# Kernel optimization log

Hardware: AMD Instinct MI355X
Metric: run time of the kernel (lower is better)

Reference implementation:

```python
import jax, jax.numpy as jnp
import numpy as np

N_NODES = 100000
N_EDGES = 1600000
IN_C, HID, OUT_C = 128, 128, 64
BN_EPS = 1e-5


def gcn_conv(x, W, b, src, dst):
    # PyG GCNConv(normalize=False): linear first, then sum-aggregate over edges
    m = x @ W                                   # [N, out_dim]
    agg = jax.ops.segment_sum(m[src], dst, num_segments=N_NODES)  # scatter-add by dst
    return agg + b


def batch_norm(h, gamma, beta):
    mu = jnp.mean(h, axis=0)
    var = jnp.var(h, axis=0)
    return (h - mu) * jax.lax.rsqrt(var + BN_EPS) * gamma + beta


def setup_inputs() -> dict:
    key = jax.random.key(0)
    ks = jax.random.split(key, 8)
    x = jax.random.normal(ks[0], (N_NODES, IN_C), dtype=jnp.float32)
    edge_src = jax.random.randint(ks[1], (N_EDGES,), 0, N_NODES, dtype=jnp.int32)
    edge_dst = jnp.sort(jax.random.randint(ks[2], (N_EDGES,), 0, N_NODES, dtype=jnp.int32))
    def glorot(k, shape):
        lim = float(np.sqrt(6.0 / (shape[0] + shape[1])))
        return jax.random.uniform(k, shape, jnp.float32, -lim, lim)
    return {
        "x": x, "edge_src": edge_src, "edge_dst": edge_dst,
        "W0": glorot(ks[3], (IN_C, HID)), "b0": jnp.zeros((HID,), jnp.float32),
        "W1": glorot(ks[4], (HID, HID)), "b1": jnp.zeros((HID,), jnp.float32),
        "W2": glorot(ks[5], (HID, OUT_C)), "b2": jnp.zeros((OUT_C,), jnp.float32),
        "g0": jnp.ones((HID,), jnp.float32), "be0": jnp.zeros((HID,), jnp.float32),
        "g1": jnp.ones((HID,), jnp.float32), "be1": jnp.zeros((HID,), jnp.float32),
    }


def reference(x, edge_src, edge_dst, W0, b0, W1, b1, W2, b2, g0, be0, g1, be1):
    # layer 0: conv -> BN -> residual (dims match: 128==128) -> ReLU (dropout p=0)
    h = gcn_conv(x, W0, b0, edge_src, edge_dst)
    h = batch_norm(h, g0, be0)
    h = h + x  # residual, in_channels == hidden_channels
    x1 = jax.nn.relu(h)
    # layer 1
    h = gcn_conv(x1, W1, b1, edge_src, edge_dst)
    h = batch_norm(h, g1, be1)
    h = h + x1
    x2 = jax.nn.relu(h)
    # final layer: conv only
    return gcn_conv(x2, W2, b2, edge_src, edge_dst)
```

## Files before the change

### kernel.cpp

```cpp
#include <hip/hip_runtime.h>

#define BN_EPS 1e-5f

typedef __attribute__((ext_vector_type(8))) short bf16x8;
typedef __attribute__((ext_vector_type(4))) float f32x4;

__device__ __forceinline__ short f2bf(float f) {
    union { float f; unsigned u; } v; v.f = f;
    unsigned r = (v.u + 0x7fffu + ((v.u >> 16) & 1u)) >> 16;
    return (short)r;
}
__device__ __forceinline__ float bflo(unsigned d) {
    union { unsigned u; float f; } v; v.u = d << 16; return v.f;
}
__device__ __forceinline__ float bfhi(unsigned d) {
    union { unsigned u; float f; } v; v.u = d & 0xffff0000u; return v.f;
}

__global__ __launch_bounds__(256) void build_off_k(const int* __restrict__ dst,
                                                   int* __restrict__ off, int E, int N) {
    int i = blockIdx.x * 256 + threadIdx.x;
    if (i > E) return;
    int cur  = (i < E) ? dst[i] : N;
    int prev = (i == 0) ? -1 : dst[i - 1];
    for (int n = prev + 1; n <= cur; ++n) off[n] = i;
}

__global__ void zero_k(float* p, int n) {
    int i = blockIdx.x * blockDim.x + threadIdx.x;
    if (i < n) p[i] = 0.f;
}

__global__ __launch_bounds__(256) void wtrans_k(const float* __restrict__ W,
                                                short* __restrict__ Wt, int K, int C) {
    int i = blockIdx.x * 256 + threadIdx.x;
    if (i >= K * C) return;
    int c = i / K, k = i % K;
    Wt[i] = f2bf(W[k * C + c]);
}

template <int OUTC, int MODE>
__global__ __launch_bounds__(256) void mgemm_k(const void* __restrict__ Xp,
                                               const short* __restrict__ Wt,
                                               short* __restrict__ M,
                                               const float* __restrict__ ss,
                                               const void* __restrict__ Rp,
                                               short* __restrict__ X1, int N) {
    constexpr int NR = OUTC / 16;
    __shared__ short sW[OUTC][136];

    const int tid = threadIdx.x;
    for (int q = tid; q < OUTC * 16; q += 256) {
        int r = q >> 4, s = q & 15;
        *(int4*)&sW[r][s * 8] = ((const int4*)Wt)[q];
    }
    __syncthreads();

    const int wave = tid >> 6, lane = tid & 63;
    const int lr = lane & 15, lg = lane >> 4;
    const int row0 = blockIdx.x * 128 + wave * 32;

    f32x4 acc[2][NR];
    #pragma unroll
    for (int m = 0; m < 2; ++m)
        #pragma unroll
        for (int n = 0; n < NR; ++n) acc[m][n] = (f32x4){0.f, 0.f, 0.f, 0.f};

    #pragma unroll
    for (int kk = 0; kk < 4; ++kk) {
        bf16x8 a[2];
        const int ch0 = kk * 32 + lg * 8;
        #pragma unroll
        for (int m = 0; m < 2; ++m) {
            int row = row0 + m * 16 + lr;
            float v[8] = {0.f, 0.f, 0.f, 0.f, 0.f, 0.f, 0.f, 0.f};
            if (row < N) {
                if constexpr (MODE == 0) {
                    const float4* p = (const float4*)((const float*)Xp + (size_t)row * 128 + ch0);
                    float4 h0 = p[0], h1 = p[1];
                    v[0] = h0.x; v[1] = h0.y; v[2] = h0.z; v[3] = h0.w;
                    v[4] = h1.x; v[5] = h1.y; v[6] = h1.z; v[7] = h1.w;
                } else {
                    int4 hb = *(const int4*)((const short*)Xp + (size_t)row * 128 + ch0);
                    v[0] = bflo(hb.x); v[1] = bfhi(hb.x);
                    v[2] = bflo(hb.y); v[3] = bfhi(hb.y);
                    v[4] = bflo(hb.z); v[5] = bfhi(hb.z);
                    v[6] = bflo(hb.w); v[7] = bfhi(hb.w);
                    float4 sc0 = *(const float4*)&ss[ch0];
                    float4 sc1 = *(const float4*)&ss[ch0 + 4];
                    float4 sh0 = *(const float4*)&ss[128 + ch0];
                    float4 sh1 = *(const float4*)&ss[128 + ch0 + 4];
                    float sc[8] = {sc0.x, sc0.y, sc0.z, sc0.w, sc1.x, sc1.y, sc1.z, sc1.w};
                    float sh[8] = {sh0.x, sh0.y, sh0.z, sh0.w, sh1.x, sh1.y, sh1.z, sh1.w};
                    float r[8];
                    if constexpr (MODE == 1) {
                        const float4* rp = (const float4*)((const float*)Rp + (size_t)row * 128 + ch0);
                        float4 r0 = rp[0], r1 = rp[1];
                        r[0] = r0.x; r[1] = r0.y; r[2] = r0.z; r[3] = r0.w;
                        r[4] = r1.x; r[5] = r1.y; r[6] = r1.z; r[7] = r1.w;
                    } else {
                        int4 rb = *(const int4*)((const short*)Rp + (size_t)row * 128 + ch0);
                        r[0] = bflo(rb.x); r[1] = bfhi(rb.x);
                        r[2] = bflo(rb.y); r[3] = bfhi(rb.y);
                        r[4] = bflo(rb.z); r[5] = bfhi(rb.z);
                        r[6] = bflo(rb.w); r[7] = bfhi(rb.w);
                    }
                    #pragma unroll
                    for (int k = 0; k < 8; ++k)
                        v[k] = fmaxf(fmaf(v[k], sc[k], sh[k]) + r[k], 0.f);
                }
            }
            #pragma unroll
            for (int k = 0; k < 8; ++k) a[m][k] = f2bf(v[k]);
            if constexpr (MODE == 1) {
                if (row < N) *(bf16x8*)&X1[(size_t)row * 128 + ch0] = a[m];
            }
        }
        #pragma unroll
        for (int n = 0; n < NR; ++n) {
            bf16x8 b = *(const bf16x8*)&sW[n * 16 + lr][kk * 32 + lg * 8];
            acc[0][n] = __builtin_amdgcn_mfma_f32_16x16x32_bf16(a[0], b, acc[0][n], 0, 0, 0);
            acc[1][n] = __builtin_amdgcn_mfma_f32_16x16x32_bf16(a[1], b, acc[1][n], 0, 0, 0);
        }
    }

    #pragma unroll
    for (int m = 0; m < 2; ++m)
        #pragma unroll
        for (int r = 0; r < 4; ++r) {
            int row = row0 + m * 16 + lg * 4 + r;
            if (row < N) {
                #pragma unroll
                for (int n = 0; n < NR; ++n)
                    M[(size_t)row * OUTC + n * 16 + lr] = f2bf(acc[m][n][r]);
            }
        }
}

template <int C, bool OUTBF>
__global__ __launch_bounds__(256) void agg_k(const short* __restrict__ M,
                                             const int* __restrict__ src,
                                             const int* __restrict__ off,
                                             const float* __restrict__ bias,
                                             void* __restrict__ Hp, int N) {
    const int lane = threadIdx.x & 63;
    const int node = blockIdx.x * 4 + (threadIdx.x >> 6);
    if (node >= N) return;
    const int e0 = off[node], e1 = off[node + 1];

    if constexpr (C == 128) {
        const unsigned* __restrict__ M32 = (const unsigned*)M;
        float2 acc = make_float2(0.f, 0.f);
        for (int base = e0; base < e1; base += 64) {
            int e = base + lane;
            int s = (e < e1) ? src[e] : 0;
            int cnt = min(64, e1 - base);
            int i = 0;
            for (; i + 4 <= cnt; i += 4) {
                int s0 = __shfl(s, i),     s1 = __shfl(s, i + 1);
                int s2 = __shfl(s, i + 2), s3 = __shfl(s, i + 3);
                unsigned d0 = M32[(size_t)s0 * 64 + lane];
                unsigned d1 = M32[(size_t)s1 * 64 + lane];
                unsigned d2 = M32[(size_t)s2 * 64 + lane];
                unsigned d3 = M32[(size_t)s3 * 64 + lane];
                acc.x += (bflo(d0) + bflo(d1)) + (bflo(d2) + bflo(d3));
                acc.y += (bfhi(d0) + bfhi(d1)) + (bfhi(d2) + bfhi(d3));
            }
            for (; i < cnt; ++i) {
                int si = __shfl(s, i);
                unsigned d = M32[(size_t)si * 64 + lane];
                acc.x += bflo(d); acc.y += bfhi(d);
            }
        }
        float2 bv = *(const float2*)&bias[lane * 2];
        float hx = acc.x + bv.x, hy = acc.y + bv.y;
        if constexpr (OUTBF) {
            unsigned d = (unsigned)(unsigned short)f2bf(hx)
                       | ((unsigned)(unsigned short)f2bf(hy) << 16);
            ((unsigned*)Hp)[(size_t)node * 64 + lane] = d;
        } else {
            *(float2*)((float*)Hp + (size_t)node * 128 + lane * 2) = make_float2(hx, hy);
        }
    } else {
        const unsigned short* __restrict__ M16 = (const unsigned short*)M;
        float acc = 0.f;
        for (int base = e0; base < e1; base += 64) {
            int e = base + lane;
            int s = (e < e1) ? src[e] : 0;
            int cnt = min(64, e1 - base);
            int i = 0;
            for (; i + 4 <= cnt; i += 4) {
                int s0 = __shfl(s, i),     s1 = __shfl(s, i + 1);
                int s2 = __shfl(s, i + 2), s3 = __shfl(s, i + 3);
                float v0 = bflo((unsigned)M16[(size_t)s0 * 64 + lane]);
                float v1 = bflo((unsigned)M16[(size_t)s1 * 64 + lane]);
                float v2 = bflo((unsigned)M16[(size_t)s2 * 64 + lane]);
                float v3 = bflo((unsigned)M16[(size_t)s3 * 64 + lane]);
                acc += (v0 + v1) + (v2 + v3);
            }
            for (; i < cnt; ++i) {
                int si = __shfl(s, i);
                acc += bflo((unsigned)M16[(size_t)si * 64 + lane]);
            }
        }
        ((float*)Hp)[(size_t)node * 64 + lane] = acc + bias[lane];
    }
}

__global__ __launch_bounds__(256) void stats_k(const short* __restrict__ Hb,
                                               float* __restrict__ stats, int N) {
    const int lane = threadIdx.x & 63, wave = threadIdx.x >> 6;
    const unsigned* __restrict__ H32 = (const unsigned*)Hb;
    float2 sum = make_float2(0.f, 0.f), sq = make_float2(0.f, 0.f);
    for (int r = blockIdx.x * 4 + wave; r < N; r += gridDim.x * 4) {
        unsigned d = H32[(size_t)r * 64 + lane];
        float lo = bflo(d), hi = bfhi(d);
        sum.x += lo; sum.y += hi;
        sq.x = fmaf(lo, lo, sq.x); sq.y = fmaf(hi, hi, sq.y);
    }
    __shared__ float sL[4][256];
    sL[wave][lane * 2]           = sum.x;
    sL[wave][lane * 2 + 1]       = sum.y;
    sL[wave][128 + lane * 2]     = sq.x;
    sL[wave][128 + lane * 2 + 1] = sq.y;
    __syncthreads();
    int tid = threadIdx.x;
    float v = sL[0][tid] + sL[1][tid] + sL[2][tid] + sL[3][tid];
    atomicAdd(&stats[tid], v);
}

__global__ void bnfin_k(const float* __restrict__ stats, const float* __restrict__ gamma,
                        const float* __restrict__ beta, float* __restrict__ ss, float invN) {
    int c = threadIdx.x;
    float mu  = stats[c] * invN;
    float var = fmaf(-mu, mu, stats[128 + c] * invN);
    float sc  = gamma[c] * rsqrtf(var + BN_EPS);
    ss[c]       = sc;
    ss[128 + c] = fmaf(-mu, sc, beta[c]);
}

extern "C" void kernel_launch(void* const* d_in, const int* in_sizes, int n_in,
                              void* d_out, int out_size, void* d_ws, size_t ws_size,
                              hipStream_t stream) {
    const float* x   = (const float*)d_in[0];
    const int*   src = (const int*)d_in[1];
    const int*   dst = (const int*)d_in[2];
    const float* W0  = (const float*)d_in[3];
    const float* b0  = (const float*)d_in[4];
    const float* W1  = (const float*)d_in[5];
    const float* b1  = (const float*)d_in[6];
    const float* W2  = (const float*)d_in[7];
    const float* b2  = (const float*)d_in[8];
    const float* g0  = (const float*)d_in[9];
    const float* be0 = (const float*)d_in[10];
    const float* g1  = (const float*)d_in[11];
    const float* be1 = (const float*)d_in[12];
    float* out = (float*)d_out;

    const int N = in_sizes[0] / 128;
    const int E = in_sizes[1];

    char*  ws   = (char*)d_ws;
    size_t bufH = (size_t)N * 128 * sizeof(short);
    short* Mb = (short*)(ws);
    short* Hb = (short*)(ws + bufH);
    short* X1 = (short*)(ws + 2 * bufH);
    size_t p  = 3 * bufH;
    p = (p + 255) & ~(size_t)255;
    int*   off = (int*)(ws + p);
    p += ((size_t)(N + 1) * sizeof(int) + 255) & ~(size_t)255;
    float* stats0 = (float*)(ws + p); p += 1024;
    float* stats1 = (float*)(ws + p); p += 1024;
    float* ss0    = (float*)(ws + p); p += 1024;
    float* ss1    = (float*)(ws + p); p += 1024;
    short* Wt0    = (short*)(ws + p); p += 128 * 128 * 2;
    short* Wt1    = (short*)(ws + p); p += 128 * 128 * 2;
    short* Wt2    = (short*)(ws + p); p += 128 * 64 * 2;

    const dim3 blk(256);
    const int gGemm  = (N + 127) / 128;
    const int gAgg   = (N + 3) / 4;
    const int gStats = 2048;
    const float invN = 1.f / (float)N;

    zero_k<<<2, blk, 0, stream>>>(stats0, 512);
    wtrans_k<<<64, blk, 0, stream>>>(W0, Wt0, 128, 128);
    wtrans_k<<<64, blk, 0, stream>>>(W1, Wt1, 128, 128);
    wtrans_k<<<32, blk, 0, stream>>>(W2, Wt2, 128, 64);
    build_off_k<<<(E + 256) / 256, blk, 0, stream>>>(dst, off, E, N);

    mgemm_k<128, 0><<<gGemm, blk, 0, stream>>>(x, Wt0, Mb, nullptr, nullptr, nullptr, N);
    agg_k<128, true><<<gAgg, blk, 0, stream>>>(Mb, src, off, b0, Hb, N);
    stats_k<<<gStats, blk, 0, stream>>>(Hb, stats0, N);
    bnfin_k<<<1, 128, 0, stream>>>(stats0, g0, be0, ss0, invN);

    mgemm_k<128, 1><<<gGemm, blk, 0, stream>>>(Hb, Wt1, Mb, ss0, x, X1, N);
    agg_k<128, true><<<gAgg, blk, 0, stream>>>(Mb, src, off, b1, Hb, N);
    stats_k<<<gStats, blk, 0, stream>>>(Hb, stats1, N);
    bnfin_k<<<1, 128, 0, stream>>>(stats1, g1, be1, ss1, invN);

    mgemm_k<64, 2><<<gGemm, blk, 0, stream>>>(Hb, Wt2, Mb, ss1, X1, nullptr, N);
    agg_k<64, false><<<gAgg, blk, 0, stream>>>(Mb, src, off, b2, out, N);
}
```

Measured before the change: 370.1 us.

## Fuse prologue kernels, fold BN finalize into GEMM, deepen gather loads in aggregation

Merges the offset build, weight transposes and stats zeroing into one prologue launch, and computes the BatchNorm scale/shift inside each GEMM block instead of in a separate single-block kernel, removing several small launches. The aggregation kernels now issue 16 independent gathers per batch, using clamped indices with zero weights in place of a scalar remainder loop. The 64-channel aggregation uses two half-waves on different edges with 32-bit loads and then combines them. This increases memory-level parallelism in the gather, at the cost of redundant masked loads on low-degree nodes and repeated BN finalize work in every GEMM block.

```diff
diff --git a/kernel.cpp b/kernel.cpp
--- a/kernel.cpp
+++ b/kernel.cpp
@@ -17,39 +17,74 @@
     union { unsigned u; float f; } v; v.u = d & 0xffff0000u; return v.f;
 }
 
-__global__ __launch_bounds__(256) void build_off_k(const int* __restrict__ dst,
-                                                   int* __restrict__ off, int E, int N) {
-    int i = blockIdx.x * 256 + threadIdx.x;
-    if (i > E) return;
-    int cur  = (i < E) ? dst[i] : N;
-    int prev = (i == 0) ? -1 : dst[i - 1];
-    for (int n = prev + 1; n <= cur; ++n) off[n] = i;
-}
-
-__global__ void zero_k(float* p, int n) {
-    int i = blockIdx.x * blockDim.x + threadIdx.x;
-    if (i < n) p[i] = 0.f;
-}
-
-__global__ __launch_bounds__(256) void wtrans_k(const float* __restrict__ W,
-                                                short* __restrict__ Wt, int K, int C) {
-    int i = blockIdx.x * 256 + threadIdx.x;
-    if (i >= K * C) return;
-    int c = i / K, k = i % K;
-    Wt[i] = f2bf(W[k * C + c]);
+__global__ __launch_bounds__(256) void prologue_k(const int* __restrict__ dst,
+                                                  int* __restrict__ off, int E, int N,
+                                                  const float* __restrict__ W0, short* __restrict__ Wt0,
+                                                  const float* __restrict__ W1, short* __restrict__ Wt1,
+                                                  const float* __restrict__ W2, short* __restrict__ Wt2,
+                                                  float* __restrict__ stats) {
+    int b = blockIdx.x;
+    const int nbOff = (E + 256) / 256;
+    if (b < nbOff) {
+        int i = b * 256 + threadIdx.x;
+        if (i > E) return;
+        int cur  = (i < E) ? dst[i] : N;
+        int prev = (i == 0) ? -1 : dst[i - 1];
+        for (int n = prev + 1; n <= cur; ++n) off[n] = i;
+        return;
+    }
+    b -= nbOff;
+    if (b < 64) {
+        int i = b * 256 + threadIdx.x;
+        int c = i / 128, k = i % 128;
+        Wt0[i] = f2bf(W0[k * 128 + c]);
+        return;
+    }
+    b -= 64;
+    if (b < 64) {
+        int i = b * 256 + threadIdx.x;
+        int c = i / 128, k = i % 128;
+        Wt1[i] = f2bf(W1[k * 128 + c]);
+        return;
+    }
+    b -= 64;
+    if (b < 32) {
+        int i = b * 256 + threadIdx.x;
+        int c = i / 128, k = i % 128;
+        Wt2[i] = f2bf(W2[k * 64 + c]);
+        return;
+    }
+    b -= 32;
+    if (b == 0) {
+        stats[threadIdx.x] = 0.f;
+        stats[threadIdx.x + 256] = 0.f;
+    }
 }
 
 template <int OUTC, int MODE>
 __global__ __launch_bounds__(256) void mgemm_k(const void* __restrict__ Xp,
                                                const short* __restrict__ Wt,
                                                short* __restrict__ M,
-                                               const float* __restrict__ ss,
+                                               const float* __restrict__ stats,
+                                               const float* __restrict__ gamma,
+                                               const float* __restrict__ beta,
+                                               float invN,
                                                const void* __restrict__ Rp,
                                                short* __restrict__ X1, int N) {
     constexpr int NR = OUTC / 16;
     __shared__ short sW[OUTC][136];
+    __shared__ float sSS[256];
 
     const int tid = threadIdx.x;
+    if constexpr (MODE != 0) {
+        if (tid < 128) {
+            float mu  = stats[tid] * invN;
+            float var = fmaf(-mu, mu, stats[128 + tid] * invN);
+            float sc  = gamma[tid] * rsqrtf(var + BN_EPS);
+            sSS[tid]       = sc;
+            sSS[128 + tid] = fmaf(-mu, sc, beta[tid]);
+        }
+    }
     for (int q = tid; q < OUTC * 16; q += 256) {
         int r = q >> 4, s = q & 15;
         *(int4*)&sW[r][s * 8] = ((const int4*)Wt)[q];
@@ -86,12 +121,12 @@
                     v[2] = bflo(hb.y); v[3] = bfhi(hb.y);
                     v[4] = bflo(hb.z); v[5] = bfhi(hb.z);
                     v[6] = bflo(hb.w); v[7] = bfhi(hb.w);
-                    float4 sc0 = *(const float4*)&ss[ch0];
-                    float4 sc1 = *(const float4*)&ss[ch0 + 4];
-                    float4 sh0 = *(const float4*)&ss[128 + ch0];
-                    float4 sh1 = *(const float4*)&ss[128 + ch0 + 4];
-                    float sc[8] = {sc0.x, sc0.y, sc0.z, sc0.w, sc1.x, sc1.y, sc1.z, sc1.w};
-                    float sh[8] = {sh0.x, sh0.y, sh0.z, sh0.w, sh1.x, sh1.y, sh1.z, sh1.w};
+                    float sc[8], sh[8];
+                    #pragma unroll
+                    for (int k = 0; k < 8; ++k) {
+                        sc[k] = sSS[ch0 + k];
+                        sh[k] = sSS[128 + ch0 + k];
+                    }
                     float r[8];
                     if constexpr (MODE == 1) {
                         const float4* rp = (const float4*)((const float*)Rp + (size_t)row * 128 + ch0);
@@ -137,73 +172,92 @@
         }
 }
 
-template <int C, bool OUTBF>
-__global__ __launch_bounds__(256) void agg_k(const short* __restrict__ M,
-                                             const int* __restrict__ src,
-                                             const int* __restrict__ off,
-                                             const float* __restrict__ bias,
-                                             void* __restrict__ Hp, int N) {
+template <bool OUTBF>
+__global__ __launch_bounds__(256) void agg128_k(const short* __restrict__ M,
+                                                const int* __restrict__ src,
+                                                const int* __restrict__ off,
+                                                const float* __restrict__ bias,
+                                                void* __restrict__ Hp, int N) {
     const int lane = threadIdx.x & 63;
     const int node = blockIdx.x * 4 + (threadIdx.x >> 6);
     if (node >= N) return;
     const int e0 = off[node], e1 = off[node + 1];
-
-    if constexpr (C == 128) {
-        const unsigned* __restrict__ M32 = (const unsigned*)M;
-        float2 acc = make_float2(0.f, 0.f);
-        for (int base = e0; base < e1; base += 64) {
-            int e = base + lane;
-            int s = (e < e1) ? src[e] : 0;
-            int cnt = min(64, e1 - base);
-            int i = 0;
-            for (; i + 4 <= cnt; i += 4) {
-                int s0 = __shfl(s, i),     s1 = __shfl(s, i + 1);
-                int s2 = __shfl(s, i + 2), s3 = __shfl(s, i + 3);
-                unsigned d0 = M32[(size_t)s0 * 64 + lane];
-                unsigned d1 = M32[(size_t)s1 * 64 + lane];
-                unsigned d2 = M32[(size_t)s2 * 64 + lane];
-                unsigned d3 = M32[(size_t)s3 * 64 + lane];
-                acc.x += (bflo(d0) + bflo(d1)) + (bflo(d2) + bflo(d3));
-                acc.y += (bfhi(d0) + bfhi(d1)) + (bfhi(d2) + bfhi(d3));
-            }
-            for (; i < cnt; ++i) {
-                int si = __shfl(s, i);
-                unsigned d = M32[(size_t)si * 64 + lane];
-                acc.x += bflo(d); acc.y += bfhi(d);
-            }
-        }
-        float2 bv = *(const float2*)&bias[lane * 2];
-        float hx = acc.x + bv.x, hy = acc.y + bv.y;
-        if constexpr (OUTBF) {
-            unsigned d = (unsigned)(unsigned short)f2bf(hx)
-                       | ((unsigned)(unsigned short)f2bf(hy) << 16);
-            ((unsigned*)Hp)[(size_t)node * 64 + lane] = d;
-        } else {
-            *(float2*)((float*)Hp + (size_t)node * 128 + lane * 2) = make_float2(hx, hy);
-        }
+    const unsigned* __restrict__ M32 = (const unsigned*)M;
+
+    float accx = 0.f, accy = 0.f;
+    for (int base = e0; base < e1; base += 64) {
+        const int cnt = min(64, e1 - base);
+        int e = base + lane;
+        int s = (e < e1) ? src[e] : 0;
+        for (int j = 0; j < cnt; j += 16) {
+            unsigned d[16];
+            float wt[16];
+            #pragma unroll
+            for (int i = 0; i < 16; ++i) {
+                int idx = j + i;
+                int ii  = idx < cnt ? idx : cnt - 1;
+                int si  = __shfl(s, ii);
+                d[i]  = M32[(size_t)si * 64 + lane];
+                wt[i] = idx < cnt ? 1.f : 0.f;
+            }
+            #pragma unroll
+            for (int i = 0; i < 16; ++i) {
+                accx = fmaf(wt[i], bflo(d[i]), accx);
+                accy = fmaf(wt[i], bfhi(d[i]), accy);
+            }
+        }
+    }
+    float2 bv = *(const float2*)&bias[lane * 2];
+    float hx = accx + bv.x, hy = accy + bv.y;
+    if constexpr (OUTBF) {
+        unsigned d = (unsigned)(unsigned short)f2bf(hx)
+                   | ((unsigned)(unsigned short)f2bf(hy) << 16);
+        ((unsigned*)Hp)[(size_t)node * 64 + lane] = d;
     } else {
-        const unsigned short* __restrict__ M16 = (const unsigned short*)M;
-        float acc = 0.f;
-        for (int base = e0; base < e1; base += 64) {
-            int e = base + lane;
-            int s = (e < e1) ? src[e] : 0;
-            int cnt = min(64, e1 - base);
-            int i = 0;
-            for (; i + 4 <= cnt; i += 4) {
-                int s0 = __shfl(s, i),     s1 = __shfl(s, i + 1);
-                int s2 = __shfl(s, i + 2), s3 = __shfl(s, i + 3);
-                float v0 = bflo((unsigned)M16[(size_t)s0 * 64 + lane]);
-                float v1 = bflo((unsigned)M16[(size_t)s1 * 64 + lane]);
-                float v2 = bflo((unsigned)M16[(size_t)s2 * 64 + lane]);
-                float v3 = bflo((unsigned)M16[(size_t)s3 * 64 + lane]);
-                acc += (v0 + v1) + (v2 + v3);
-            }
-            for (; i < cnt; ++i) {
-                int si = __shfl(s, i);
-                acc += bflo((unsigned)M16[(size_t)si * 64 + lane]);
-            }
-        }
-        ((float*)Hp)[(size_t)node * 64 + lane] = acc + bias[lane];
+        *(float2*)((float*)Hp + (size_t)node * 128 + lane * 2) = make_float2(hx, hy);
+    }
+}
+
+__global__ __launch_bounds__(256) void agg64_k(const short* __restrict__ M,
+                                               const int* __restrict__ src,
+                                               const int* __restrict__ off,
+                                               const float* __restrict__ bias,
+                                               float* __restrict__ out, int N) {
+    const int lane = threadIdx.x & 63;
+    const int node = blockIdx.x * 4 + (threadIdx.x >> 6);
+    if (node >= N) return;
+    const int e0 = off[node], e1 = off[node + 1];
+    const unsigned* __restrict__ M32 = (const unsigned*)M;
+    const int e2 = lane >> 5, c = lane & 31;
+
+    float accx = 0.f, accy = 0.f;
+    for (int base = e0; base < e1; base += 64) {
+        const int cnt = min(64, e1 - base);
+        int e = base + lane;
+        int s = (e < e1) ? src[e] : 0;
+        for (int j = 0; j < cnt; j += 16) {
+            unsigned d[8];
+            float wt[8];
+            #pragma unroll
+            for (int i = 0; i < 8; ++i) {
+                int idx = j + i * 2 + e2;
+                int ii  = idx < cnt ? idx : cnt - 1;
+                int si  = __shfl(s, ii);
+                d[i]  = M32[(size_t)si * 32 + c];
+                wt[i] = idx < cnt ? 1.f : 0.f;
+            }
+            #pragma unroll
+            for (int i = 0; i < 8; ++i) {
+                accx = fmaf(wt[i], bflo(d[i]), accx);
+                accy = fmaf(wt[i], bfhi(d[i]), accy);
+            }
+        }
+    }
+    accx += __shfl_xor(accx, 32);
+    accy += __shfl_xor(accy, 32);
+    if (e2 == 0) {
+        float2 bv = *(const float2*)&bias[c * 2];
+        *(float2*)&out[(size_t)node * 64 + c * 2] = make_float2(accx + bv.x, accy + bv.y);
     }
 }
 
@@ -227,16 +281,6 @@
     int tid = threadIdx.x;
     float v = sL[0][tid] + sL[1][tid] + sL[2][tid] + sL[3][tid];
     atomicAdd(&stats[tid], v);
-}
-
-__global__ void bnfin_k(const float* __restrict__ stats, const float* __restrict__ gamma,
-                        const float* __restrict__ beta, float* __restrict__ ss, float invN) {
-    int c = threadIdx.x;
-    float mu  = stats[c] * invN;
-    float var = fmaf(-mu, mu, stats[128 + c] * invN);
-    float sc  = gamma[c] * rsqrtf(var + BN_EPS);
-    ss[c]       = sc;
-    ss[128 + c] = fmaf(-mu, sc, beta[c]);
 }
 
 extern "C" void kernel_launch(void* const* d_in, const int* in_sizes, int n_in,
@@ -271,34 +315,29 @@
     p += ((size_t)(N + 1) * sizeof(int) + 255) & ~(size_t)255;
     float* stats0 = (float*)(ws + p); p += 1024;
     float* stats1 = (float*)(ws + p); p += 1024;
-    float* ss0    = (float*)(ws + p); p += 1024;
-    float* ss1    = (float*)(ws + p); p += 1024;
     short* Wt0    = (short*)(ws + p); p += 128 * 128 * 2;
     short* Wt1    = (short*)(ws + p); p += 128 * 128 * 2;
     short* Wt2    = (short*)(ws + p); p += 128 * 64 * 2;
 
     const dim3 blk(256);
+    const int nbOff  = (E + 256) / 256;
+    const int gPro   = nbOff + 64 + 64 + 32 + 1;
     const int gGemm  = (N + 127) / 128;
     const int gAgg   = (N + 3) / 4;
     const int gStats = 2048;
     const float invN = 1.f / (float)N;
 
-    zero_k<<<2, blk, 0, stream>>>(stats0, 512);
-    wtrans_k<<<64, blk, 0, stream>>>(W0, Wt0, 128, 128);
-    wtrans_k<<<64, blk, 0, stream>>>(W1, Wt1, 128, 128);
-    wtrans_k<<<32, blk, 0, stream>>>(W2, Wt2, 128, 64);
-    build_off_k<<<(E + 256) / 256, blk, 0, stream>>>(dst, off, E, N);
-
-    mgemm_k<128, 0><<<gGemm, blk, 0, stream>>>(x, Wt0, Mb, nullptr, nullptr, nullptr, N);
-    agg_k<128, true><<<gAgg, blk, 0, stream>>>(Mb, src, off, b0, Hb, N);
+    prologue_k<<<gPro, blk, 0, stream>>>(dst, off, E, N, W0, Wt0, W1, Wt1, W2, Wt2, stats0);
+
+    mgemm_k<128, 0><<<gGemm, blk, 0, stream>>>(x, Wt0, Mb, nullptr, nullptr, nullptr, 0.f,
+                                               nullptr, nullptr, N);
+    agg128_k<true><<<gAgg, blk, 0, stream>>>(Mb, src, off, b0, Hb, N);
     stats_k<<<gStats, blk, 0, stream>>>(Hb, stats0, N);
-    bnfin_k<<<1, 128, 0, stream>>>(stats0, g0, be0, ss0, invN);
-
-    mgemm_k<128, 1><<<gGemm, blk, 0, stream>>>(Hb, Wt1, Mb, ss0, x, X1, N);
-    agg_k<128, true><<<gAgg, blk, 0, stream>>>(Mb, src, off, b1, Hb, N);
+
+    mgemm_k<128, 1><<<gGemm, blk, 0, stream>>>(Hb, Wt1, Mb, stats0, g0, be0, invN, x, X1, N);
+    agg128_k<true><<<gAgg, blk, 0, stream>>>(Mb, src, off, b1, Hb, N);
     stats_k<<<gStats, blk, 0, stream>>>(Hb, stats1, N);
-    bnfin_k<<<1, 128, 0, stream>>>(stats1, g1, be1, ss1, invN);
-
-    mgemm_k<64, 2><<<gGemm, blk, 0, stream>>>(Hb, Wt2, Mb, ss1, X1, nullptr, N);
-    agg_k<64, false><<<gAgg, blk, 0, stream>>>(Mb, src, off, b2, out, N);
-}
+
+    mgemm_k<64, 2><<<gGemm, blk, 0, stream>>>(Hb, Wt2, Mb, stats1, g1, be1, invN, X1, nullptr, N);
+    agg64_k<<<gAgg, blk, 0, stream>>>(Mb, src, off, b2, out, N);
+}
```

After: 343.8 us. -7.1%, faster.
